# Performance work log

Hardware: AMD Instinct MI355X
Metric: run time of the kernel (lower is better)

The kernel has to match this reference:

```python
import jax, jax.numpy as jnp
import numpy as np

B, P, D = 8, 1024, 1024
H, N = 16, 64  # num_heads, head_dim


def setup_inputs() -> dict:
    key = jax.random.key(0)
    k1, k2, k3 = jax.random.split(key, 3)
    inputs = jax.random.normal(k1, (B, P, D), dtype=jnp.float32)
    # Keras 'random_normal' initializer: stddev 0.05
    w_qkv = jax.random.normal(k2, (H, 3, D, N), dtype=jnp.float32) * 0.05
    w_o = jax.random.normal(k3, (N * H, D), dtype=jnp.float32) * 0.05
    return {"inputs": inputs, "w_qkv": w_qkv, "w_o": w_o}


def reference(inputs, w_qkv, w_o):
    # Per-head QKV projection: [b,p,d] x [h,3,d,n] -> [b,h,3,p,n]
    proj = jnp.einsum('bpv,havn->bhapn', inputs, w_qkv)
    q = proj[:, :, 0]  # [b,h,p,n]
    k = proj[:, :, 1]
    v = proj[:, :, 2]
    head_dim = q.shape[-1]
    scale = 1.0 / jnp.sqrt(jnp.asarray(head_dim, dtype=jnp.float32))
    scores = jnp.einsum('bhqn,bhkn->bhqk', q, k) * scale  # [b,h,p,p]
    attn = jax.nn.softmax(scores, axis=-1)
    out = jnp.einsum('bhqk,bhkn->bhqn', attn, v)  # [b,h,p,n]
    # concat heads along feature dim: [b,p,h*n]
    b, h, p, n = out.shape
    concat = out.transpose(0, 2, 1, 3).reshape(b, p, h * n)
    return jnp.einsum('bpi,ij->bpj', concat, w_o)  # [b,p,d_model]
```

## Files before the change

kernel.cpp:

```cpp
#include <hip/hip_runtime.h>
#include <stdint.h>

typedef _Float16 f16;
typedef __attribute__((ext_vector_type(2))) _Float16 f16x2;
typedef __attribute__((ext_vector_type(4))) _Float16 f16x4;
typedef __attribute__((ext_vector_type(8))) _Float16 f16x8;
typedef __attribute__((ext_vector_type(2))) __fp16 h16x2;
typedef __attribute__((ext_vector_type(4))) float f32x4;
typedef __attribute__((ext_vector_type(4))) uint32_t u32x4;

__device__ __forceinline__ void gload_lds16(const void* g, void* l) {
  __builtin_amdgcn_global_load_lds(
      (__attribute__((address_space(1))) void*)const_cast<void*>(g),
      (__attribute__((address_space(3))) void*)l, 16, 0, 0);
}


__global__ void convert_x(const float* __restrict__ in, f16* __restrict__ out) {
  int i = blockIdx.x * 256 + threadIdx.x;
  float4 v = ((const float4*)in)[i];
  f16x4 hv;
  hv[0] = (f16)v.x; hv[1] = (f16)v.y; hv[2] = (f16)v.z; hv[3] = (f16)v.w;
  ((f16x4*)out)[i] = hv;
}

__global__ void transpose_wqkv(const float* __restrict__ in, f16* __restrict__ out) {
  __shared__ float tile[64][65];
  int s = blockIdx.x >> 4;
  int vt = blockIdx.x & 15;
  int hh = s / 3, a = s - hh * 3;
  int tx = threadIdx.x & 63, ty = threadIdx.x >> 6;
#pragma unroll
  for (int i = 0; i < 16; i++) {
    int r = i * 4 + ty;
    tile[r][tx] = in[((size_t)(s * 1024 + vt * 64 + r)) * 64 + tx];
  }
  __syncthreads();
#pragma unroll
  for (int i = 0; i < 16; i++) {
    int n = i * 4 + ty;
    out[((size_t)(a * 1024 + hh * 64 + n)) * 1024 + vt * 64 + tx] = (f16)tile[tx][n];
  }
}

__global__ void transpose_wo(const float* __restrict__ in, f16* __restrict__ out) {
  __shared__ float tile[64][65];
  int rt = blockIdx.x >> 4, ct = blockIdx.x & 15;
  int tx = threadIdx.x & 63, ty = threadIdx.x >> 6;
#pragma unroll
  for (int i = 0; i < 16; i++) {
    int r = i * 4 + ty;
    tile[r][tx] = in[((size_t)(rt * 64 + r)) * 1024 + ct * 64 + tx];
  }
  __syncthreads();
#pragma unroll
  for (int i = 0; i < 16; i++) {
    int j = i * 4 + ty;
    out[((size_t)(ct * 64 + j)) * 1024 + rt * 64 + tx] = (f16)tile[tx][j];
  }
}

template <int OUTMODE>
__global__ __launch_bounds__(256, 4) void gemm_kernel(
    const f16* __restrict__ A, const f16* __restrict__ BT, void* __restrict__ out,
    void* __restrict__ out2, int M, int N, int K) {
  __shared__ __align__(16) f16 As[128][64];
  __shared__ __align__(16) f16 Bs[128][64];
  const int t = threadIdx.x;
  const int lane = t & 63, wave = t >> 6;
  const int lr = lane & 15, lg = lane >> 4;
  const int wm = wave >> 1, wn = wave & 1;
  const int nTN = N >> 7;
  const int bm = blockIdx.x / nTN, bn = blockIdx.x % nTN;
  const f16* Ab = A + (size_t)bm * 128 * K;
  const f16* Bb = BT + (size_t)bn * 128 * K;

  const f32x4 zero4 = {0.f, 0.f, 0.f, 0.f};
  f32x4 acc[4][4];
#pragma unroll
  for (int m = 0; m < 4; m++)
#pragma unroll
    for (int n = 0; n < 4; n++) acc[m][n] = zero4;

  for (int k0 = 0; k0 < K; k0 += 64) {
    __syncthreads();
#pragma unroll
    for (int i = 0; i < 4; i++) {
      int q = wave * 4 + i;
      int u = q * 64 + lane;
      int r = u >> 3, j = u & 7;
      gload_lds16(Ab + (size_t)r * K + k0 + ((j ^ (r & 7)) << 3),
                  (char*)&As[0][0] + q * 1024);
      gload_lds16(Bb + (size_t)r * K + k0 + ((j ^ (r & 7)) << 3),
                  (char*)&Bs[0][0] + q * 1024);
    }
    __syncthreads();
#pragma unroll
    for (int half = 0; half < 2; half++) {
      f16x8 af[4], bf[4];
#pragma unroll
      for (int m = 0; m < 4; m++) {
        int r = wm * 64 + m * 16 + lr;
        af[m] = *(const f16x8*)&As[r][((half * 4 + lg) ^ (r & 7)) << 3];
      }
#pragma unroll
      for (int n = 0; n < 4; n++) {
        int r = wn * 64 + n * 16 + lr;
        bf[n] = *(const f16x8*)&Bs[r][((half * 4 + lg) ^ (r & 7)) << 3];
      }
#pragma unroll
      for (int m = 0; m < 4; m++)
#pragma unroll
        for (int n = 0; n < 4; n++)
          acc[m][n] = __builtin_amdgcn_mfma_f32_16x16x32_f16(af[m], bf[n], acc[m][n], 0, 0, 0);
    }
  }

  const int r0 = bm * 128 + wm * 64;
  const int c0 = bn * 128 + wn * 64;
  if (OUTMODE == 2 && bn >= 16) {
    f16* VT = (f16*)out2;
    const int bb = bm >> 3;
#pragma unroll
    for (int m = 0; m < 4; m++) {
      int pl = (r0 + m * 16 + lg * 4) & 1023;
      int pl2 = (pl & 992) | ((pl & 12) << 1) | ((pl & 16) >> 2);
#pragma unroll
      for (int n = 0; n < 4; n++) {
        int vcol = c0 - 2048 + n * 16 + lr;
        f16x4 pv;
#pragma unroll
        for (int i = 0; i < 4; i++) pv[i] = (f16)acc[m][n][i];
        *(f16x4*)&VT[((size_t)(bb * 16 + (vcol >> 6)) * 64 + (vcol & 63)) * 1024 + pl2] = pv;
      }
    }
  } else {
#pragma unroll
    for (int m = 0; m < 4; m++)
#pragma unroll
      for (int n = 0; n < 4; n++)
#pragma unroll
        for (int i = 0; i < 4; i++) {
          int gr = r0 + m * 16 + lg * 4 + i;
          int gc = c0 + n * 16 + lr;
          if (OUTMODE == 1)
            ((float*)out)[(size_t)gr * N + gc] = acc[m][n][i];
          else
            ((f16*)out)[(size_t)gr * N + gc] = (f16)acc[m][n][i];
        }
  }
}

__global__ __launch_bounds__(256, 4) void attn_kernel(
    const f16* __restrict__ QKV, const f16* __restrict__ VT, f16* __restrict__ C) {
  __shared__ __align__(16) f16 smem[16384];

  const int t = threadIdx.x, lane = t & 63, wave = t >> 6;
  const int lr = lane & 15, lg = lane >> 4;
  const int pt = blockIdx.x, bh = blockIdx.y;
  const int b = bh >> 4, h = bh & 15;
  const int p0 = pt * 128;

  const f16* Qg = QKV + ((size_t)(b * 1024 + p0)) * 3072 + h * 64;
  const f16* Kg = QKV + ((size_t)(b * 1024)) * 3072 + 1024 + h * 64;
  const f16* Vg = VT + (size_t)bh * 64 * 1024;

#pragma unroll
  for (int i = 0; i < 4; i++) {
    int q = wave * 4 + i;
    int u = q * 64 + lane;
    int r = u >> 3, j = u & 7;
    gload_lds16(Qg + (size_t)r * 3072 + ((j ^ (r & 7)) << 3), (char*)smem + q * 1024);
  }
  __syncthreads();

  const f16 qscale = (f16)0.180336878f;
  f16x8 qa[2][2];
#pragma unroll
  for (int m = 0; m < 2; m++)
#pragma unroll
    for (int hh = 0; hh < 2; hh++) {
      int r = wave * 32 + m * 16 + lr;
      f16x8 v = *(const f16x8*)&smem[(size_t)r * 64 + (((hh * 4 + lg) ^ (lr & 7)) << 3)];
#pragma unroll
      for (int e = 0; e < 8; e++) v[e] *= qscale;
      qa[m][hh] = v;
    }
  __syncthreads();

  auto STAGE = [&](int kc, int cur) {
#pragma unroll
    for (int i = 0; i < 2; i++) {
      int q = wave * 2 + i;
      int u = q * 64 + lane;
      int r = u >> 3, j = u & 7;
      gload_lds16(Kg + (size_t)(kc * 64 + r) * 3072 + ((j ^ (r & 7)) << 3),
                  (char*)smem + cur * 16384 + q * 1024);
      gload_lds16(Vg + (size_t)r * 1024 + kc * 64 + ((j ^ (r & 7)) << 3),
                  (char*)smem + cur * 16384 + 8192 + q * 1024);
    }
  };

  STAGE(0, 0);
  STAGE(1, 1);
  asm volatile("s_waitcnt vmcnt(4)" ::: "memory");
  asm volatile("s_barrier" ::: "memory");

  const f32x4 zero4 = {0.f, 0.f, 0.f, 0.f};
  f32x4 o[2][4], o_l[2];
#pragma unroll
  for (int m = 0; m < 2; m++) {
    o_l[m] = zero4;
#pragma unroll
    for (int n = 0; n < 4; n++) o[m][n] = zero4;
  }
  float mrun[2] = {0.f, 0.f};
  const f16x8 ones8 = {(f16)1.f, (f16)1.f, (f16)1.f, (f16)1.f,
                       (f16)1.f, (f16)1.f, (f16)1.f, (f16)1.f};

#pragma unroll 1
  for (int kc = 0; kc < 16; kc++) {
    const int cur = kc & 1;
    const int kB = cur * 8192;
    const char* vB = (const char*)smem + cur * 16384 + 8192;

    f32x4 s[2][4];
#pragma unroll
    for (int m = 0; m < 2; m++) {
      f32x4 init = {-mrun[m], -mrun[m], -mrun[m], -mrun[m]};
#pragma unroll
      for (int kb = 0; kb < 4; kb++) s[m][kb] = init;
    }
    __builtin_amdgcn_s_setprio(1);
#pragma unroll
    for (int kb = 0; kb < 4; kb++) {
      int r = kb * 16 + lr;
      f16x8 kf0 = *(const f16x8*)&smem[kB + (size_t)r * 64 + ((lg ^ (lr & 7)) << 3)];
      f16x8 kf1 = *(const f16x8*)&smem[kB + (size_t)r * 64 + (((4 + lg) ^ (lr & 7)) << 3)];
#pragma unroll
      for (int m = 0; m < 2; m++) {
        s[m][kb] = __builtin_amdgcn_mfma_f32_16x16x32_f16(kf0, qa[m][0], s[m][kb], 0, 0, 0);
        s[m][kb] = __builtin_amdgcn_mfma_f32_16x16x32_f16(kf1, qa[m][1], s[m][kb], 0, 0, 0);
      }
    }
    __builtin_amdgcn_s_setprio(0);

    f16x8 pa8[2][2];
#pragma unroll
    for (int m = 0; m < 2; m++) {
      float mx = fmaxf(fmaxf(fmaxf(s[m][0][0], s[m][0][1]), fmaxf(s[m][0][2], s[m][0][3])),
                       fmaxf(fmaxf(s[m][1][0], s[m][1][1]), fmaxf(s[m][1][2], s[m][1][3])));
      mx = fmaxf(mx, fmaxf(fmaxf(fmaxf(s[m][2][0], s[m][2][1]), fmaxf(s[m][2][2], s[m][2][3])),
                           fmaxf(fmaxf(s[m][3][0], s[m][3][1]), fmaxf(s[m][3][2], s[m][3][3]))));
      mx = fmaxf(mx, __shfl_xor(mx, 16));
      mx = fmaxf(mx, __shfl_xor(mx, 32));
      if (__any(mx > 4.328085f)) {
        float delta = fmaxf(mx, 0.f);
        mrun[m] += delta;
        float alpha = exp2f(-delta);
#pragma unroll
        for (int kb = 0; kb < 4; kb++)
#pragma unroll
          for (int i = 0; i < 4; i++) s[m][kb][i] -= delta;
#pragma unroll
        for (int i = 0; i < 4; i++) {
          float ai = __shfl(alpha, (lane & 48) | (lg * 4 + i));
          o_l[m][i] *= ai;
#pragma unroll
          for (int n = 0; n < 4; n++) o[m][n][i] *= ai;
        }
      }
#pragma unroll
      for (int j = 0; j < 2; j++) {
        uint32_t w0, w1, w2, w3;
        w0 = __builtin_bit_cast(uint32_t, __builtin_amdgcn_cvt_pkrtz(exp2f(s[m][2 * j][0]), exp2f(s[m][2 * j][1])));
        w1 = __builtin_bit_cast(uint32_t, __builtin_amdgcn_cvt_pkrtz(exp2f(s[m][2 * j][2]), exp2f(s[m][2 * j][3])));
        w2 = __builtin_bit_cast(uint32_t, __builtin_amdgcn_cvt_pkrtz(exp2f(s[m][2 * j + 1][0]), exp2f(s[m][2 * j + 1][1])));
        w3 = __builtin_bit_cast(uint32_t, __builtin_amdgcn_cvt_pkrtz(exp2f(s[m][2 * j + 1][2]), exp2f(s[m][2 * j + 1][3])));
        u32x4 ww = {w0, w1, w2, w3};
        pa8[m][j] = __builtin_bit_cast(f16x8, ww);
      }
    }

    __builtin_amdgcn_s_setprio(1);
#pragma unroll
    for (int j = 0; j < 2; j++) {
      o_l[0] = __builtin_amdgcn_mfma_f32_16x16x32_f16(pa8[0][j], ones8, o_l[0], 0, 0, 0);
      o_l[1] = __builtin_amdgcn_mfma_f32_16x16x32_f16(pa8[1][j], ones8, o_l[1], 0, 0, 0);
#pragma unroll
      for (int n = 0; n < 4; n++) {
        int rv = n * 16 + lr;
        f16x8 vb = *(const f16x8*)(vB + (size_t)rv * 128 + (((4 * j + lg) ^ (lr & 7)) << 4));
        o[0][n] = __builtin_amdgcn_mfma_f32_16x16x32_f16(pa8[0][j], vb, o[0][n], 0, 0, 0);
        o[1][n] = __builtin_amdgcn_mfma_f32_16x16x32_f16(pa8[1][j], vb, o[1][n], 0, 0, 0);
      }
    }
    __builtin_amdgcn_s_setprio(0);

    asm volatile("s_waitcnt lgkmcnt(0)\n\ts_barrier" ::: "memory");
    if (kc + 2 < 16) {
      STAGE(kc + 2, cur);
      asm volatile("s_waitcnt vmcnt(4)" ::: "memory");
    } else {
      asm volatile("s_waitcnt vmcnt(0)" ::: "memory");
    }
    asm volatile("s_barrier" ::: "memory");
  }

#pragma unroll
  for (int m = 0; m < 2; m++)
#pragma unroll
    for (int i = 0; i < 4; i++) {
      float li = 1.f / o_l[m][i];
      int prow = p0 + wave * 32 + m * 16 + lg * 4 + i;
#pragma unroll
      for (int n = 0; n < 4; n++) {
        int col = h * 64 + n * 16 + lr;
        C[((size_t)(b * 1024 + prow)) * 1024 + col] = (f16)(o[m][n][i] * li);
      }
    }
}

extern "C" void kernel_launch(void* const* d_in, const int* in_sizes, int n_in,
                              void* d_out, int out_size, void* d_ws, size_t ws_size,
                              hipStream_t stream) {
  const float* X = (const float*)d_in[0];
  const float* Wqkv = (const float*)d_in[1];
  const float* Wo = (const float*)d_in[2];
  float* Y = (float*)d_out;

  f16* ws = (f16*)d_ws;
  f16* X16 = ws;
  f16* WqkvT = ws + 8388608;
  f16* WoT = ws + 11534336;
  f16* QKV = ws + 12582912;
  f16* VT = (f16*)d_out;

  convert_x<<<8192, 256, 0, stream>>>(X, X16);
  transpose_wqkv<<<768, 256, 0, stream>>>(Wqkv, WqkvT);
  transpose_wo<<<256, 256, 0, stream>>>(Wo, WoT);
  gemm_kernel<2><<<64 * 24, 256, 0, stream>>>(X16, WqkvT, QKV, VT, 8192, 3072, 1024);
  attn_kernel<<<dim3(8, 128), 256, 0, stream>>>(QKV, VT, X16 );
  gemm_kernel<1><<<64 * 8, 256, 0, stream>>>(X16 , WoT, Y, nullptr, 8192, 1024, 1024);
}
```

Before: 174.3 us.

## Switch attention kernel to 32x32x16 MFMA with transposed S and staged output stores

Rewrites the attention inner loop to compute S^T with 32x32x16 MFMAs, so each wave holds one 32-query tile whose softmax max reduction needs only one cross-lane shuffle and no per-row alpha shuffles. P is fed directly as the B operand of the PV and row-sum MFMAs, and the V-transpose permutation in the projection GEMM is changed to match the new operand layout. The epilogue stages the output through LDS and writes 16-byte coalesced rows instead of scalar f16 stores. Launch bounds occupancy drops from 4 to 3 to leave room for the larger accumulator register footprint.

```diff
diff --git a/kernel.cpp b/kernel.cpp
--- a/kernel.cpp
+++ b/kernel.cpp
@@ -7,6 +7,7 @@
 typedef __attribute__((ext_vector_type(8))) _Float16 f16x8;
 typedef __attribute__((ext_vector_type(2))) __fp16 h16x2;
 typedef __attribute__((ext_vector_type(4))) float f32x4;
+typedef __attribute__((ext_vector_type(16))) float f32x16;
 typedef __attribute__((ext_vector_type(4))) uint32_t u32x4;
 
 __device__ __forceinline__ void gload_lds16(const void* g, void* l) {
@@ -124,7 +125,7 @@
 #pragma unroll
     for (int m = 0; m < 4; m++) {
       int pl = (r0 + m * 16 + lg * 4) & 1023;
-      int pl2 = (pl & 992) | ((pl & 12) << 1) | ((pl & 16) >> 2);
+      int pl2 = (pl & ~12) | ((pl & 4) << 1) | ((pl & 8) >> 1);
 #pragma unroll
       for (int n = 0; n < 4; n++) {
         int vcol = c0 - 2048 + n * 16 + lr;
@@ -151,12 +152,12 @@
   }
 }
 
-__global__ __launch_bounds__(256, 4) void attn_kernel(
+__global__ __launch_bounds__(256, 3) void attn_kernel(
     const f16* __restrict__ QKV, const f16* __restrict__ VT, f16* __restrict__ C) {
   __shared__ __align__(16) f16 smem[16384];
 
   const int t = threadIdx.x, lane = t & 63, wave = t >> 6;
-  const int lr = lane & 15, lg = lane >> 4;
+  const int q = lane & 31, hi = lane >> 5, q7 = lane & 7;
   const int pt = blockIdx.x, bh = blockIdx.y;
   const int b = bh >> 4, h = bh & 15;
   const int p0 = pt * 128;
@@ -167,37 +168,38 @@
 
 #pragma unroll
   for (int i = 0; i < 4; i++) {
-    int q = wave * 4 + i;
-    int u = q * 64 + lane;
+    int qn = wave * 4 + i;
+    int u = qn * 64 + lane;
     int r = u >> 3, j = u & 7;
-    gload_lds16(Qg + (size_t)r * 3072 + ((j ^ (r & 7)) << 3), (char*)smem + q * 1024);
+    gload_lds16(Qg + (size_t)r * 3072 + ((j ^ (r & 7)) << 3), (char*)smem + qn * 1024);
   }
   __syncthreads();
 
   const f16 qscale = (f16)0.180336878f;
-  f16x8 qa[2][2];
-#pragma unroll
-  for (int m = 0; m < 2; m++)
-#pragma unroll
-    for (int hh = 0; hh < 2; hh++) {
-      int r = wave * 32 + m * 16 + lr;
-      f16x8 v = *(const f16x8*)&smem[(size_t)r * 64 + (((hh * 4 + lg) ^ (lr & 7)) << 3)];
+  f16x8 qB[4];
+  {
+    int rq = wave * 32 + q;
+#pragma unroll
+    for (int w = 0; w < 4; w++) {
+      int cb = (2 * w + hi) ^ q7;
+      f16x8 v = *(const f16x8*)&smem[(size_t)rq * 64 + (cb << 3)];
 #pragma unroll
       for (int e = 0; e < 8; e++) v[e] *= qscale;
-      qa[m][hh] = v;
-    }
+      qB[w] = v;
+    }
+  }
   __syncthreads();
 
   auto STAGE = [&](int kc, int cur) {
 #pragma unroll
     for (int i = 0; i < 2; i++) {
-      int q = wave * 2 + i;
-      int u = q * 64 + lane;
+      int qn = wave * 2 + i;
+      int u = qn * 64 + lane;
       int r = u >> 3, j = u & 7;
       gload_lds16(Kg + (size_t)(kc * 64 + r) * 3072 + ((j ^ (r & 7)) << 3),
-                  (char*)smem + cur * 16384 + q * 1024);
+                  (char*)smem + cur * 16384 + qn * 1024);
       gload_lds16(Vg + (size_t)r * 1024 + kc * 64 + ((j ^ (r & 7)) << 3),
-                  (char*)smem + cur * 16384 + 8192 + q * 1024);
+                  (char*)smem + cur * 16384 + 8192 + qn * 1024);
     }
   };
 
@@ -206,15 +208,10 @@
   asm volatile("s_waitcnt vmcnt(4)" ::: "memory");
   asm volatile("s_barrier" ::: "memory");
 
-  const f32x4 zero4 = {0.f, 0.f, 0.f, 0.f};
-  f32x4 o[2][4], o_l[2];
-#pragma unroll
-  for (int m = 0; m < 2; m++) {
-    o_l[m] = zero4;
-#pragma unroll
-    for (int n = 0; n < 4; n++) o[m][n] = zero4;
-  }
-  float mrun[2] = {0.f, 0.f};
+  f32x16 o0, o1, ol;
+#pragma unroll
+  for (int e = 0; e < 16; e++) { o0[e] = 0.f; o1[e] = 0.f; ol[e] = 0.f; }
+  float mrun = 0.f;
   const f16x8 ones8 = {(f16)1.f, (f16)1.f, (f16)1.f, (f16)1.f,
                        (f16)1.f, (f16)1.f, (f16)1.f, (f16)1.f};
 
@@ -222,77 +219,86 @@
   for (int kc = 0; kc < 16; kc++) {
     const int cur = kc & 1;
     const int kB = cur * 8192;
-    const char* vB = (const char*)smem + cur * 16384 + 8192;
-
-    f32x4 s[2][4];
-#pragma unroll
-    for (int m = 0; m < 2; m++) {
-      f32x4 init = {-mrun[m], -mrun[m], -mrun[m], -mrun[m]};
-#pragma unroll
-      for (int kb = 0; kb < 4; kb++) s[m][kb] = init;
-    }
+    const int vB = cur * 8192 + 4096;
+
+    f32x16 s0, s1;
+#pragma unroll
+    for (int e = 0; e < 16; e++) { s0[e] = -mrun; s1[e] = -mrun; }
     __builtin_amdgcn_s_setprio(1);
 #pragma unroll
-    for (int kb = 0; kb < 4; kb++) {
-      int r = kb * 16 + lr;
-      f16x8 kf0 = *(const f16x8*)&smem[kB + (size_t)r * 64 + ((lg ^ (lr & 7)) << 3)];
-      f16x8 kf1 = *(const f16x8*)&smem[kB + (size_t)r * 64 + (((4 + lg) ^ (lr & 7)) << 3)];
-#pragma unroll
-      for (int m = 0; m < 2; m++) {
-        s[m][kb] = __builtin_amdgcn_mfma_f32_16x16x32_f16(kf0, qa[m][0], s[m][kb], 0, 0, 0);
-        s[m][kb] = __builtin_amdgcn_mfma_f32_16x16x32_f16(kf1, qa[m][1], s[m][kb], 0, 0, 0);
-      }
+    for (int w = 0; w < 4; w++) {
+      int cb = ((2 * w + hi) ^ q7) << 3;
+      f16x8 kf0 = *(const f16x8*)&smem[kB + (size_t)q * 64 + cb];
+      f16x8 kf1 = *(const f16x8*)&smem[kB + (size_t)(32 + q) * 64 + cb];
+      s0 = __builtin_amdgcn_mfma_f32_32x32x16_f16(kf0, qB[w], s0, 0, 0, 0);
+      s1 = __builtin_amdgcn_mfma_f32_32x32x16_f16(kf1, qB[w], s1, 0, 0, 0);
     }
     __builtin_amdgcn_s_setprio(0);
 
-    f16x8 pa8[2][2];
-#pragma unroll
-    for (int m = 0; m < 2; m++) {
-      float mx = fmaxf(fmaxf(fmaxf(s[m][0][0], s[m][0][1]), fmaxf(s[m][0][2], s[m][0][3])),
-                       fmaxf(fmaxf(s[m][1][0], s[m][1][1]), fmaxf(s[m][1][2], s[m][1][3])));
-      mx = fmaxf(mx, fmaxf(fmaxf(fmaxf(s[m][2][0], s[m][2][1]), fmaxf(s[m][2][2], s[m][2][3])),
-                           fmaxf(fmaxf(s[m][3][0], s[m][3][1]), fmaxf(s[m][3][2], s[m][3][3]))));
-      mx = fmaxf(mx, __shfl_xor(mx, 16));
-      mx = fmaxf(mx, __shfl_xor(mx, 32));
-      if (__any(mx > 4.328085f)) {
-        float delta = fmaxf(mx, 0.f);
-        mrun[m] += delta;
-        float alpha = exp2f(-delta);
-#pragma unroll
-        for (int kb = 0; kb < 4; kb++)
-#pragma unroll
-          for (int i = 0; i < 4; i++) s[m][kb][i] -= delta;
-#pragma unroll
-        for (int i = 0; i < 4; i++) {
-          float ai = __shfl(alpha, (lane & 48) | (lg * 4 + i));
-          o_l[m][i] *= ai;
-#pragma unroll
-          for (int n = 0; n < 4; n++) o[m][n][i] *= ai;
-        }
-      }
-#pragma unroll
-      for (int j = 0; j < 2; j++) {
-        uint32_t w0, w1, w2, w3;
-        w0 = __builtin_bit_cast(uint32_t, __builtin_amdgcn_cvt_pkrtz(exp2f(s[m][2 * j][0]), exp2f(s[m][2 * j][1])));
-        w1 = __builtin_bit_cast(uint32_t, __builtin_amdgcn_cvt_pkrtz(exp2f(s[m][2 * j][2]), exp2f(s[m][2 * j][3])));
-        w2 = __builtin_bit_cast(uint32_t, __builtin_amdgcn_cvt_pkrtz(exp2f(s[m][2 * j + 1][0]), exp2f(s[m][2 * j + 1][1])));
-        w3 = __builtin_bit_cast(uint32_t, __builtin_amdgcn_cvt_pkrtz(exp2f(s[m][2 * j + 1][2]), exp2f(s[m][2 * j + 1][3])));
-        u32x4 ww = {w0, w1, w2, w3};
-        pa8[m][j] = __builtin_bit_cast(f16x8, ww);
-      }
+    float mx = fmaxf(s0[0], s0[1]);
+#pragma unroll
+    for (int e = 2; e < 16; e++) mx = fmaxf(mx, s0[e]);
+#pragma unroll
+    for (int e = 0; e < 16; e++) mx = fmaxf(mx, s1[e]);
+    mx = fmaxf(mx, __shfl_xor(mx, 32));
+    if (__any(mx > 4.328085f)) {
+      float delta = fmaxf(mx, 0.f);
+      mrun += delta;
+      float alpha = exp2f(-delta);
+#pragma unroll
+      for (int e = 0; e < 16; e++) {
+        s0[e] -= delta; s1[e] -= delta;
+        o0[e] *= alpha; o1[e] *= alpha; ol[e] *= alpha;
+      }
+    }
+
+    f16x8 pb00, pb01, pb10, pb11;
+    {
+      u32x4 ww;
+      ww[0] = __builtin_bit_cast(uint32_t, __builtin_amdgcn_cvt_pkrtz(exp2f(s0[0]), exp2f(s0[1])));
+      ww[1] = __builtin_bit_cast(uint32_t, __builtin_amdgcn_cvt_pkrtz(exp2f(s0[2]), exp2f(s0[3])));
+      ww[2] = __builtin_bit_cast(uint32_t, __builtin_amdgcn_cvt_pkrtz(exp2f(s0[4]), exp2f(s0[5])));
+      ww[3] = __builtin_bit_cast(uint32_t, __builtin_amdgcn_cvt_pkrtz(exp2f(s0[6]), exp2f(s0[7])));
+      pb00 = __builtin_bit_cast(f16x8, ww);
+      ww[0] = __builtin_bit_cast(uint32_t, __builtin_amdgcn_cvt_pkrtz(exp2f(s0[8]), exp2f(s0[9])));
+      ww[1] = __builtin_bit_cast(uint32_t, __builtin_amdgcn_cvt_pkrtz(exp2f(s0[10]), exp2f(s0[11])));
+      ww[2] = __builtin_bit_cast(uint32_t, __builtin_amdgcn_cvt_pkrtz(exp2f(s0[12]), exp2f(s0[13])));
+      ww[3] = __builtin_bit_cast(uint32_t, __builtin_amdgcn_cvt_pkrtz(exp2f(s0[14]), exp2f(s0[15])));
+      pb01 = __builtin_bit_cast(f16x8, ww);
+      ww[0] = __builtin_bit_cast(uint32_t, __builtin_amdgcn_cvt_pkrtz(exp2f(s1[0]), exp2f(s1[1])));
+      ww[1] = __builtin_bit_cast(uint32_t, __builtin_amdgcn_cvt_pkrtz(exp2f(s1[2]), exp2f(s1[3])));
+      ww[2] = __builtin_bit_cast(uint32_t, __builtin_amdgcn_cvt_pkrtz(exp2f(s1[4]), exp2f(s1[5])));
+      ww[3] = __builtin_bit_cast(uint32_t, __builtin_amdgcn_cvt_pkrtz(exp2f(s1[6]), exp2f(s1[7])));
+      pb10 = __builtin_bit_cast(f16x8, ww);
+      ww[0] = __builtin_bit_cast(uint32_t, __builtin_amdgcn_cvt_pkrtz(exp2f(s1[8]), exp2f(s1[9])));
+      ww[1] = __builtin_bit_cast(uint32_t, __builtin_amdgcn_cvt_pkrtz(exp2f(s1[10]), exp2f(s1[11])));
+      ww[2] = __builtin_bit_cast(uint32_t, __builtin_amdgcn_cvt_pkrtz(exp2f(s1[12]), exp2f(s1[13])));
+      ww[3] = __builtin_bit_cast(uint32_t, __builtin_amdgcn_cvt_pkrtz(exp2f(s1[14]), exp2f(s1[15])));
+      pb11 = __builtin_bit_cast(f16x8, ww);
     }
 
     __builtin_amdgcn_s_setprio(1);
-#pragma unroll
-    for (int j = 0; j < 2; j++) {
-      o_l[0] = __builtin_amdgcn_mfma_f32_16x16x32_f16(pa8[0][j], ones8, o_l[0], 0, 0, 0);
-      o_l[1] = __builtin_amdgcn_mfma_f32_16x16x32_f16(pa8[1][j], ones8, o_l[1], 0, 0, 0);
-#pragma unroll
-      for (int n = 0; n < 4; n++) {
-        int rv = n * 16 + lr;
-        f16x8 vb = *(const f16x8*)(vB + (size_t)rv * 128 + (((4 * j + lg) ^ (lr & 7)) << 4));
-        o[0][n] = __builtin_amdgcn_mfma_f32_16x16x32_f16(pa8[0][j], vb, o[0][n], 0, 0, 0);
-        o[1][n] = __builtin_amdgcn_mfma_f32_16x16x32_f16(pa8[1][j], vb, o[1][n], 0, 0, 0);
+    ol = __builtin_amdgcn_mfma_f32_32x32x16_f16(ones8, pb00, ol, 0, 0, 0);
+    ol = __builtin_amdgcn_mfma_f32_32x32x16_f16(ones8, pb01, ol, 0, 0, 0);
+    ol = __builtin_amdgcn_mfma_f32_32x32x16_f16(ones8, pb10, ol, 0, 0, 0);
+    ol = __builtin_amdgcn_mfma_f32_32x32x16_f16(ones8, pb11, ol, 0, 0, 0);
+#pragma unroll
+    for (int nb = 0; nb < 2; nb++) {
+      const int rA = 32 * nb + q;
+      f16x8 vf00 = *(const f16x8*)&smem[vB + (size_t)rA * 64 + (((0 + hi) ^ q7) << 3)];
+      f16x8 vf01 = *(const f16x8*)&smem[vB + (size_t)rA * 64 + (((2 + hi) ^ q7) << 3)];
+      f16x8 vf10 = *(const f16x8*)&smem[vB + (size_t)rA * 64 + (((4 + hi) ^ q7) << 3)];
+      f16x8 vf11 = *(const f16x8*)&smem[vB + (size_t)rA * 64 + (((6 + hi) ^ q7) << 3)];
+      if (nb == 0) {
+        o0 = __builtin_amdgcn_mfma_f32_32x32x16_f16(vf00, pb00, o0, 0, 0, 0);
+        o0 = __builtin_amdgcn_mfma_f32_32x32x16_f16(vf01, pb01, o0, 0, 0, 0);
+        o0 = __builtin_amdgcn_mfma_f32_32x32x16_f16(vf10, pb10, o0, 0, 0, 0);
+        o0 = __builtin_amdgcn_mfma_f32_32x32x16_f16(vf11, pb11, o0, 0, 0, 0);
+      } else {
+        o1 = __builtin_amdgcn_mfma_f32_32x32x16_f16(vf00, pb00, o1, 0, 0, 0);
+        o1 = __builtin_amdgcn_mfma_f32_32x32x16_f16(vf01, pb01, o1, 0, 0, 0);
+        o1 = __builtin_amdgcn_mfma_f32_32x32x16_f16(vf10, pb10, o1, 0, 0, 0);
+        o1 = __builtin_amdgcn_mfma_f32_32x32x16_f16(vf11, pb11, o1, 0, 0, 0);
       }
     }
     __builtin_amdgcn_s_setprio(0);
@@ -307,18 +313,32 @@
     asm volatile("s_barrier" ::: "memory");
   }
 
-#pragma unroll
-  for (int m = 0; m < 2; m++)
+  {
+    float li = 1.f / ol[0];
+    const int row = wave * 32 + q;
+    const int px = q7 << 3;
+#pragma unroll
+    for (int rp = 0; rp < 8; rp++) {
+      int r = 2 * rp;
+      int n0 = (r & 3) + 8 * (r >> 2) + 4 * hi;
+      uint32_t w0 = __builtin_bit_cast(uint32_t,
+          __builtin_amdgcn_cvt_pkrtz(o0[r] * li, o0[r + 1] * li));
+      uint32_t w1 = __builtin_bit_cast(uint32_t,
+          __builtin_amdgcn_cvt_pkrtz(o1[r] * li, o1[r + 1] * li));
+      *(uint32_t*)&smem[(size_t)row * 64 + (n0 ^ px)] = w0;
+      *(uint32_t*)&smem[(size_t)row * 64 + ((n0 + 32) ^ px)] = w1;
+    }
+  }
+  __syncthreads();
+  {
+    const int c = t & 7;
 #pragma unroll
     for (int i = 0; i < 4; i++) {
-      float li = 1.f / o_l[m][i];
-      int prow = p0 + wave * 32 + m * 16 + lg * 4 + i;
-#pragma unroll
-      for (int n = 0; n < 4; n++) {
-        int col = h * 64 + n * 16 + lr;
-        C[((size_t)(b * 1024 + prow)) * 1024 + col] = (f16)(o[m][n][i] * li);
-      }
-    }
+      int row = (t >> 3) + 32 * i;
+      f16x8 rd = *(const f16x8*)&smem[(size_t)row * 64 + ((c ^ (row & 7)) << 3)];
+      *(f16x8*)&C[((size_t)(b * 1024 + p0 + row)) * 1024 + h * 64 + c * 8] = rd;
+    }
+  }
 }
 
 extern "C" void kernel_launch(void* const* d_in, const int* in_sizes, int n_in,
```

Measured after the change: 177.1 us. No clear change (+1.6%).
